# Kernel optimization log

Hardware: AMD Instinct MI355X
Metric: run time of the kernel (lower is better)

The kernel has to match this reference:

```python
import jax, jax.numpy as jnp
import numpy as np

N, E, H, D, F_IN = 50000, 400000, 2, 128, 5
EPS = 1e-5  # BatchNorm eps

def _bn(x, gamma, beta, rm, rv):
    # eval-mode BatchNorm1d using running stats
    return (x - rm) * jax.lax.rsqrt(rv + EPS) * gamma + beta

def setup_inputs() -> dict:
    key = jax.random.key(0)
    ks = jax.random.split(key, 24)
    r = lambda i, shape, s=1.0: jax.random.normal(ks[i], shape, jnp.float32) * s
    u = lambda i, shape: jax.random.uniform(ks[i], shape, jnp.float32)
    return {
        "h": r(0, (N, F_IN)),
        "edge_index": jax.random.randint(ks[1], (2, E), 0, N),
        "edge_weight": r(2, (E, 1)),
        # BatchNorm1d(5)
        "gamma1": 1.0 + r(3, (F_IN,), 0.1), "beta1": r(4, (F_IN,), 0.1),
        "rm1": r(5, (F_IN,), 0.1), "rv1": 0.5 + u(6, (F_IN,)),
        # GATv2Conv params (lin_l, lin_r with bias; lin_edge no bias; att; out bias)
        "Wl": r(7, (F_IN, H * D), 0.2), "bl": r(8, (H * D,), 0.1),
        "Wr": r(9, (F_IN, H * D), 0.2), "br": r(10, (H * D,), 0.1),
        "We": r(11, (1, H * D), 0.2),
        "att": r(12, (H, D), 0.2),
        "bias_gat": r(13, (D,), 0.1),
        # fc1 + BatchNorm1d(128)
        "W1": r(14, (D, D), 0.08), "b1": r(15, (D,), 0.1),
        "gamma2": 1.0 + r(16, (D,), 0.1), "beta2": r(17, (D,), 0.1),
        "rm2": r(18, (D,), 0.1), "rv2": 0.5 + u(19, (D,)),
        # fc2
        "W2": r(20, (D, F_IN), 0.08), "b2": r(21, (F_IN,), 0.1),
    }

def reference(h, edge_index, edge_weight, gamma1, beta1, rm1, rv1,
              Wl, bl, Wr, br, We, att, bias_gat,
              W1, b1, gamma2, beta2, rm2, rv2, W2, b2):
    src, dst = edge_index[0], edge_index[1]
    h = _bn(h, gamma1, beta1, rm1, rv1)
    xl = (h @ Wl + bl).reshape(N, H, D)   # source transform (messages)
    xr = (h @ Wr + br).reshape(N, H, D)   # destination transform
    e = (edge_weight @ We).reshape(E, H, D)
    # GATv2: score = att . leaky_relu(x_j + x_i + edge_emb), slope 0.2
    z = jax.nn.leaky_relu(xl[src] + xr[dst] + e, 0.2)          # [E,H,D]
    logits = jnp.einsum('ehd,hd->eh', z, att)                   # [E,H]
    # segment softmax over edges sharing a destination node
    mx = jax.ops.segment_max(logits, dst, num_segments=N)       # [N,H]
    ex = jnp.exp(logits - mx[dst])
    den = jax.ops.segment_sum(ex, dst, num_segments=N)
    alpha = ex / (den[dst] + 1e-16)                             # [E,H]
    msg = xl[src] * alpha[:, :, None]                           # [E,H,D]
    ssum = jax.ops.segment_sum(msg, dst, num_segments=N)        # [N,H,D]
    cnt = jax.ops.segment_sum(jnp.ones((E,), jnp.float32), dst, num_segments=N)
    out = ssum / jnp.maximum(cnt, 1.0)[:, None, None]           # aggr='mean'
    out = out.mean(axis=1) + bias_gat                           # concat=False -> head mean
    out = out @ W1 + b1
    out = _bn(out, gamma2, beta2, rm2, rv2)
    out = jax.nn.leaky_relu(out, 0.01)
    # dropout is identity in eval mode
    out = out @ W2 + b2                                         # [N,5]
    return out
```

## Files before the change

### kernel.cpp

```cpp
#include <hip/hip_runtime.h>

#define N_NODES 50000
#define N_EDGES 400000
#define F_INP 5
#define HD 256
#define BN_EPS 1e-5f

typedef short v8s __attribute__((ext_vector_type(8)));
typedef float v4f __attribute__((ext_vector_type(4)));
typedef unsigned v4u __attribute__((ext_vector_type(4)));

#define OFF_HBN  0
#define OFF_ACC  400000
#define OFF_BPK  1200000
#define OFF_WF   1202048
#define OFF_W2P  1204096

#define PREP_BLOCKS 3125

#define DPP_ROR_F(x, n) \
    __int_as_float(__builtin_amdgcn_update_dpp(0, __float_as_int(x), 0x120 | (n), 0xF, 0xF, false))

__device__ __forceinline__ unsigned short f2bf(float f) {
    unsigned u = __float_as_uint(f);
    return (unsigned short)((u + 0x7FFFu + ((u >> 16) & 1u)) >> 16);
}
__device__ __forceinline__ unsigned pk2(float a, float b) {
    return (unsigned)f2bf(a) | ((unsigned)f2bf(b) << 16);
}

__device__ __forceinline__ float wcat(int k, int c, const float* Wl, const float* Wr,
                                      const float* We, const float* bl, const float* br) {
    if (k < 5)   return Wl[k * HD + c];
    if (k < 10)  return Wr[(k - 5) * HD + c];
    if (k == 10) return We[c];
    return bl[c] + br[c];
}

__global__ void k_prep(const float* __restrict__ h, const float* __restrict__ g1,
                       const float* __restrict__ be1, const float* __restrict__ rm1,
                       const float* __restrict__ rv1,
                       const float* __restrict__ Wl, const float* __restrict__ bl,
                       const float* __restrict__ Wr, const float* __restrict__ br,
                       const float* __restrict__ We, const float* __restrict__ att,
                       const float* __restrict__ bias_gat,
                       const float* __restrict__ W1, const float* __restrict__ b1,
                       const float* __restrict__ g2, const float* __restrict__ be2,
                       const float* __restrict__ rm2, const float* __restrict__ rv2,
                       const float* __restrict__ W2,
                       float* __restrict__ hbn8, float* __restrict__ acc,
                       unsigned* __restrict__ Bpk,
                       float* __restrict__ Wf, float* __restrict__ W2p) {
    if (blockIdx.x < PREP_BLOCKS) {
        int i = blockIdx.x * blockDim.x + threadIdx.x;
        if (i < N_NODES * 16) acc[i] = 0.f;
        if (i < N_NODES * 8) {
            int f = i & 7, n = i >> 3;
            float v = 0.f;
            if (f < F_INP) {
                float x = h[n * F_INP + f];
                v = (x - rm1[f]) * rsqrtf(rv1[f] + BN_EPS) * g1[f] + be1[f];
            }
            hbn8[i] = v;
        }
        if (i < 1024) {
            int t = i >> 6, l = i & 63;
            int g = l >> 4, c = t * 16 + (l & 15);
            unsigned d0 = 0, d1 = 0;
            if (g < 3) {
                int kb = 4 * g;
                d0 = pk2(wcat(kb + 0, c, Wl, Wr, We, bl, br),
                         wcat(kb + 1, c, Wl, Wr, We, bl, br));
                d1 = pk2(wcat(kb + 2, c, Wl, Wr, We, bl, br),
                         wcat(kb + 3, c, Wl, Wr, We, bl, br));
            }
            Bpk[(t * 64 + l) * 2 + 0] = d0;
            Bpk[(t * 64 + l) * 2 + 1] = d1;
        }
        return;
    }
    int k = blockIdx.x - PREP_BLOCKS;
    int c = threadIdx.x;
    if (c >= 128) return;
    const float* base = (k == 0) ? bl
                      : (k == 1) ? bl + 128
                      : (k < 7)  ? Wl + (k - 2) * HD
                      : (k < 12) ? Wl + (k - 7) * HD + 128
                                 : bias_gat;
    float sum = 0.f;
#pragma unroll 8
    for (int d = 0; d < 128; ++d) sum += base[d] * W1[d * 128 + c];
    if (k == 12) sum += b1[c];
    Wf[c * 16 + k] = sum;
    if (k == 0) {
        float sc = g2[c] * rsqrtf(rv2[c] + BN_EPS);
        Wf[c * 16 + 13] = sc;
        Wf[c * 16 + 14] = be2[c] - rm2[c] * sc;
        Wf[c * 16 + 15] = 0.f;
#pragma unroll
        for (int f = 0; f < 8; ++f)
            W2p[c * 8 + f] = (f < 5) ? W2[c * 5 + f] : 0.f;
    }
}

__launch_bounds__(256)
__global__ void k_edge(const float* __restrict__ hbn8, const int* __restrict__ ei,
                       const float* __restrict__ ew, const unsigned* __restrict__ Bpk,
                       const float* __restrict__ att, float* __restrict__ acc) {
    int lane = threadIdx.x & 63;
    int wv = threadIdx.x >> 6;
    int g = lane >> 4, e16 = lane & 15;

    v8s B[16];
    float AT[16];
#pragma unroll
    for (int t = 0; t < 16; ++t) {
        uint2 d = *(const uint2*)&Bpk[(t * 64 + lane) * 2];
        v4u u = {d.x, d.y, 0u, 0u};
        B[t] = __builtin_bit_cast(v8s, u);
        AT[t] = att[t * 16 + e16];
    }

    int wid = blockIdx.x * 4 + wv;
    int nw = gridDim.x * 4;
    const int NT = N_EDGES / 16;

    int j16 = e16;
    bool sact = j16 < 13;
    int kk = (j16 < 6) ? j16 - 1 : j16 - 7;
    int kc = min(max(kk, 0), 4);

    for (int tile = wid; tile < NT; tile += nw) {
        int e = tile * 16 + e16;
        int src = ei[e];
        int dst = ei[N_EDGES + e];
        float w = ew[e];
        float4 s4 = *(const float4*)&hbn8[src * 8];
        float hs4 = hbn8[src * 8 + 4];
        float4 d4 = *(const float4*)&hbn8[dst * 8];
        float hd4 = hbn8[dst * 8 + 4];

        float a0 = (g == 0) ? s4.x : (g == 1) ? hs4  : d4.w;
        float a1 = (g == 0) ? s4.y : (g == 1) ? d4.x : hd4;
        float a2 = (g == 0) ? s4.z : (g == 1) ? d4.y : w;
        float a3 = (g == 0) ? s4.w : (g == 1) ? d4.z : 1.0f;
        unsigned ua0 = (g < 3) ? pk2(a0, a1) : 0u;
        unsigned ua1 = (g < 3) ? pk2(a2, a3) : 0u;
        v4u uav = {ua0, ua1, 0u, 0u};
        v8s A = __builtin_bit_cast(v8s, uav);

        float p00 = 0.f, p01 = 0.f, p02 = 0.f, p03 = 0.f;
        float p10 = 0.f, p11 = 0.f, p12 = 0.f, p13v = 0.f;
        v4f zero = {0.f, 0.f, 0.f, 0.f};
#pragma unroll
        for (int t = 0; t < 8; ++t) {
            v4f c = __builtin_amdgcn_mfma_f32_16x16x32_bf16(A, B[t], zero, 0, 0, 0);
            p00 += AT[t] * fmaf(0.66666667f, fabsf(c[0]), c[0]);
            p01 += AT[t] * fmaf(0.66666667f, fabsf(c[1]), c[1]);
            p02 += AT[t] * fmaf(0.66666667f, fabsf(c[2]), c[2]);
            p03 += AT[t] * fmaf(0.66666667f, fabsf(c[3]), c[3]);
        }
#pragma unroll
        for (int t = 8; t < 16; ++t) {
            v4f c = __builtin_amdgcn_mfma_f32_16x16x32_bf16(A, B[t], zero, 0, 0, 0);
            p10 += AT[t] * fmaf(0.66666667f, fabsf(c[0]), c[0]);
            p11 += AT[t] * fmaf(0.66666667f, fabsf(c[1]), c[1]);
            p12 += AT[t] * fmaf(0.66666667f, fabsf(c[2]), c[2]);
            p13v += AT[t] * fmaf(0.66666667f, fabsf(c[3]), c[3]);
        }
#pragma unroll
        for (int st = 1; st <= 8; st <<= 1) {
            if (st == 1) {
                p00 += DPP_ROR_F(p00, 1); p01 += DPP_ROR_F(p01, 1);
                p02 += DPP_ROR_F(p02, 1); p03 += DPP_ROR_F(p03, 1);
                p10 += DPP_ROR_F(p10, 1); p11 += DPP_ROR_F(p11, 1);
                p12 += DPP_ROR_F(p12, 1); p13v += DPP_ROR_F(p13v, 1);
            } else if (st == 2) {
                p00 += DPP_ROR_F(p00, 2); p01 += DPP_ROR_F(p01, 2);
                p02 += DPP_ROR_F(p02, 2); p03 += DPP_ROR_F(p03, 2);
                p10 += DPP_ROR_F(p10, 2); p11 += DPP_ROR_F(p11, 2);
                p12 += DPP_ROR_F(p12, 2); p13v += DPP_ROR_F(p13v, 2);
            } else if (st == 4) {
                p00 += DPP_ROR_F(p00, 4); p01 += DPP_ROR_F(p01, 4);
                p02 += DPP_ROR_F(p02, 4); p03 += DPP_ROR_F(p03, 4);
                p10 += DPP_ROR_F(p10, 4); p11 += DPP_ROR_F(p11, 4);
                p12 += DPP_ROR_F(p12, 4); p13v += DPP_ROR_F(p13v, 4);
            } else {
                p00 += DPP_ROR_F(p00, 8); p01 += DPP_ROR_F(p01, 8);
                p02 += DPP_ROR_F(p02, 8); p03 += DPP_ROR_F(p03, 8);
                p10 += DPP_ROR_F(p10, 8); p11 += DPP_ROR_F(p11, 8);
                p12 += DPP_ROR_F(p12, 8); p13v += DPP_ROR_F(p13v, 8);
            }
        }
        float e00 = __expf(0.6f * p00), e01 = __expf(0.6f * p01);
        float e02 = __expf(0.6f * p02), e03 = __expf(0.6f * p03);
        float e10 = __expf(0.6f * p10), e11 = __expf(0.6f * p11);
        float e12 = __expf(0.6f * p12), e13 = __expf(0.6f * p13v);

        if (sact) {
#pragma unroll
            for (int it = 0; it < 4; ++it) {
                int eg = tile * 16 + 4 * g + it;
                int srcg = ei[eg];
                int deg = ei[N_EDGES + eg];
                float hsel = hbn8[srcg * 8 + kc];
                float ex0 = (it == 0) ? e00 : (it == 1) ? e01 : (it == 2) ? e02 : e03;
                float ex1 = (it == 0) ? e10 : (it == 1) ? e11 : (it == 2) ? e12 : e13;
                float base = (j16 < 6) ? ex0 : ex1;
                float v = base * hsel;
                v = (j16 == 0) ? ex0 : v;
                v = (j16 == 6) ? ex1 : v;
                v = (j16 == 12) ? 1.0f : v;
                atomicAdd(&acc[deg * 16 + j16], v);
            }
        }
    }
}

__launch_bounds__(256)
__global__ void k_mlp(const float* __restrict__ acc, const float* __restrict__ Wf,
                      const float* __restrict__ W2p, const float* __restrict__ b2,
                      float* __restrict__ out) {
    int n = blockIdx.x * blockDim.x + threadIdx.x;
    if (n >= N_NODES) return;
    const float* ar = acc + (size_t)n * 16;
    float4 A0 = *(const float4*)(ar + 0);
    float4 A1 = *(const float4*)(ar + 4);
    float4 A2 = *(const float4*)(ar + 8);
    float cnt = ar[12];
    float r0 = 1.f / (A0.x + 1e-16f);
    float r1 = 1.f / (A1.z + 1e-16f);
    float scale = 0.5f / fmaxf(cnt, 1.f);
    float s0 = scale * r0, s1 = scale * r1;
    float m0 = A0.x * s0, m1 = A1.z * s1;
    float m2 = A0.y * s0, m3 = A0.z * s0, m4 = A0.w * s0, m5 = A1.x * s0, m6 = A1.y * s0;
    float m7 = A1.w * s1, m8 = A2.x * s1, m9 = A2.y * s1, m10 = A2.z * s1, m11 = A2.w * s1;

    float o0 = 0.f, o1 = 0.f, o2 = 0.f, o3 = 0.f, o4 = 0.f;
#pragma unroll 4
    for (int c = 0; c < 128; ++c) {
        const float* wr = &Wf[c * 16];
        float a = wr[12];
        a += m0 * wr[0] + m1 * wr[1] + m2 * wr[2] + m3 * wr[3];
        a += m4 * wr[4] + m5 * wr[5] + m6 * wr[6] + m7 * wr[7];
        a += m8 * wr[8] + m9 * wr[9] + m10 * wr[10] + m11 * wr[11];
        a = fmaf(a, wr[13], wr[14]);
        a = fmaxf(a, 0.01f * a);
        const float* w2 = &W2p[c * 8];
        o0 = fmaf(a, w2[0], o0);
        o1 = fmaf(a, w2[1], o1);
        o2 = fmaf(a, w2[2], o2);
        o3 = fmaf(a, w2[3], o3);
        o4 = fmaf(a, w2[4], o4);
    }
    float* op = out + (size_t)n * 5;
    op[0] = o0 + b2[0];
    op[1] = o1 + b2[1];
    op[2] = o2 + b2[2];
    op[3] = o3 + b2[3];
    op[4] = o4 + b2[4];
}

extern "C" void kernel_launch(void* const* d_in, const int* in_sizes, int n_in,
                              void* d_out, int out_size, void* d_ws, size_t ws_size,
                              hipStream_t stream) {
    const float* h    = (const float*)d_in[0];
    const int*   ei   = (const int*)d_in[1];
    const float* ew   = (const float*)d_in[2];
    const float* g1   = (const float*)d_in[3];
    const float* be1  = (const float*)d_in[4];
    const float* rm1  = (const float*)d_in[5];
    const float* rv1  = (const float*)d_in[6];
    const float* Wl   = (const float*)d_in[7];
    const float* bl   = (const float*)d_in[8];
    const float* Wr   = (const float*)d_in[9];
    const float* br   = (const float*)d_in[10];
    const float* We   = (const float*)d_in[11];
    const float* att  = (const float*)d_in[12];
    const float* bias_gat = (const float*)d_in[13];
    const float* W1   = (const float*)d_in[14];
    const float* b1   = (const float*)d_in[15];
    const float* g2   = (const float*)d_in[16];
    const float* be2  = (const float*)d_in[17];
    const float* rm2  = (const float*)d_in[18];
    const float* rv2  = (const float*)d_in[19];
    const float* W2   = (const float*)d_in[20];
    const float* b2   = (const float*)d_in[21];

    float* ws  = (float*)d_ws;
    float* hbn = ws + OFF_HBN;
    float* acc = ws + OFF_ACC;
    unsigned* Bpk = (unsigned*)(ws + OFF_BPK);
    float* Wf  = ws + OFF_WF;
    float* W2p = ws + OFF_W2P;

    k_prep<<<PREP_BLOCKS + 13, 256, 0, stream>>>(
        h, g1, be1, rm1, rv1, Wl, bl, Wr, br, We, att, bias_gat,
        W1, b1, g2, be2, rm2, rv2, W2, hbn, acc, Bpk, Wf, W2p);
    k_edge<<<1280, 256, 0, stream>>>(hbn, ei, ew, Bpk, att, acc);
    k_mlp<<<(N_NODES + 255) / 256, 256, 0, stream>>>(acc, Wf, W2p, b2, (float*)d_out);
}
```

Before: 87.57 us.

## Replicate accumulator buffer per lane group to spread atomic contention

The per-destination accumulator is split into four replicas, and each 16-lane group of a wave atomically adds into its own copy. The MLP kernel sums the four replicas before normalising. The prep kernel now zeroes all replicas with float4 stores, and the edge kernel grid grows from 1280 to 1792 blocks. The aim is to cut same-address atomic contention, at the cost of four times the accumulator zeroing and four times the reads in the MLP.

```diff
diff --git a/kernel.cpp b/kernel.cpp
--- a/kernel.cpp
+++ b/kernel.cpp
@@ -5,6 +5,7 @@
 #define F_INP 5
 #define HD 256
 #define BN_EPS 1e-5f
+#define NREP 4
 
 typedef short v8s __attribute__((ext_vector_type(8)));
 typedef float v4f __attribute__((ext_vector_type(4)));
@@ -12,9 +13,9 @@
 
 #define OFF_HBN  0
 #define OFF_ACC  400000
-#define OFF_BPK  1200000
-#define OFF_WF   1202048
-#define OFF_W2P  1204096
+#define OFF_BPK  3600000
+#define OFF_WF   3602048
+#define OFF_W2P  3604096
 
 #define PREP_BLOCKS 3125
 
@@ -53,7 +54,8 @@
                        float* __restrict__ Wf, float* __restrict__ W2p) {
     if (blockIdx.x < PREP_BLOCKS) {
         int i = blockIdx.x * blockDim.x + threadIdx.x;
-        if (i < N_NODES * 16) acc[i] = 0.f;
+        float4 z = make_float4(0.f, 0.f, 0.f, 0.f);
+        *(float4*)&acc[(size_t)i * 4] = z;
         if (i < N_NODES * 8) {
             int f = i & 7, n = i >> 3;
             float v = 0.f;
@@ -129,6 +131,7 @@
     bool sact = j16 < 13;
     int kk = (j16 < 6) ? j16 - 1 : j16 - 7;
     int kc = min(max(kk, 0), 4);
+    float* accg = acc + (size_t)g * (N_NODES * 16);
 
     for (int tile = wid; tile < NT; tile += nw) {
         int e = tile * 16 + e16;
@@ -168,30 +171,23 @@
             p12 += AT[t] * fmaf(0.66666667f, fabsf(c[2]), c[2]);
             p13v += AT[t] * fmaf(0.66666667f, fabsf(c[3]), c[3]);
         }
-#pragma unroll
-        for (int st = 1; st <= 8; st <<= 1) {
-            if (st == 1) {
-                p00 += DPP_ROR_F(p00, 1); p01 += DPP_ROR_F(p01, 1);
-                p02 += DPP_ROR_F(p02, 1); p03 += DPP_ROR_F(p03, 1);
-                p10 += DPP_ROR_F(p10, 1); p11 += DPP_ROR_F(p11, 1);
-                p12 += DPP_ROR_F(p12, 1); p13v += DPP_ROR_F(p13v, 1);
-            } else if (st == 2) {
-                p00 += DPP_ROR_F(p00, 2); p01 += DPP_ROR_F(p01, 2);
-                p02 += DPP_ROR_F(p02, 2); p03 += DPP_ROR_F(p03, 2);
-                p10 += DPP_ROR_F(p10, 2); p11 += DPP_ROR_F(p11, 2);
-                p12 += DPP_ROR_F(p12, 2); p13v += DPP_ROR_F(p13v, 2);
-            } else if (st == 4) {
-                p00 += DPP_ROR_F(p00, 4); p01 += DPP_ROR_F(p01, 4);
-                p02 += DPP_ROR_F(p02, 4); p03 += DPP_ROR_F(p03, 4);
-                p10 += DPP_ROR_F(p10, 4); p11 += DPP_ROR_F(p11, 4);
-                p12 += DPP_ROR_F(p12, 4); p13v += DPP_ROR_F(p13v, 4);
-            } else {
-                p00 += DPP_ROR_F(p00, 8); p01 += DPP_ROR_F(p01, 8);
-                p02 += DPP_ROR_F(p02, 8); p03 += DPP_ROR_F(p03, 8);
-                p10 += DPP_ROR_F(p10, 8); p11 += DPP_ROR_F(p11, 8);
-                p12 += DPP_ROR_F(p12, 8); p13v += DPP_ROR_F(p13v, 8);
-            }
-        }
+        p00 += DPP_ROR_F(p00, 1); p01 += DPP_ROR_F(p01, 1);
+        p02 += DPP_ROR_F(p02, 1); p03 += DPP_ROR_F(p03, 1);
+        p10 += DPP_ROR_F(p10, 1); p11 += DPP_ROR_F(p11, 1);
+        p12 += DPP_ROR_F(p12, 1); p13v += DPP_ROR_F(p13v, 1);
+        p00 += DPP_ROR_F(p00, 2); p01 += DPP_ROR_F(p01, 2);
+        p02 += DPP_ROR_F(p02, 2); p03 += DPP_ROR_F(p03, 2);
+        p10 += DPP_ROR_F(p10, 2); p11 += DPP_ROR_F(p11, 2);
+        p12 += DPP_ROR_F(p12, 2); p13v += DPP_ROR_F(p13v, 2);
+        p00 += DPP_ROR_F(p00, 4); p01 += DPP_ROR_F(p01, 4);
+        p02 += DPP_ROR_F(p02, 4); p03 += DPP_ROR_F(p03, 4);
+        p10 += DPP_ROR_F(p10, 4); p11 += DPP_ROR_F(p11, 4);
+        p12 += DPP_ROR_F(p12, 4); p13v += DPP_ROR_F(p13v, 4);
+        p00 += DPP_ROR_F(p00, 8); p01 += DPP_ROR_F(p01, 8);
+        p02 += DPP_ROR_F(p02, 8); p03 += DPP_ROR_F(p03, 8);
+        p10 += DPP_ROR_F(p10, 8); p11 += DPP_ROR_F(p11, 8);
+        p12 += DPP_ROR_F(p12, 8); p13v += DPP_ROR_F(p13v, 8);
+
         float e00 = __expf(0.6f * p00), e01 = __expf(0.6f * p01);
         float e02 = __expf(0.6f * p02), e03 = __expf(0.6f * p03);
         float e10 = __expf(0.6f * p10), e11 = __expf(0.6f * p11);
@@ -211,7 +207,7 @@
                 v = (j16 == 0) ? ex0 : v;
                 v = (j16 == 6) ? ex1 : v;
                 v = (j16 == 12) ? 1.0f : v;
-                atomicAdd(&acc[deg * 16 + j16], v);
+                atomicAdd(&accg[deg * 16 + j16], v);
             }
         }
     }
@@ -223,11 +219,21 @@
                       float* __restrict__ out) {
     int n = blockIdx.x * blockDim.x + threadIdx.x;
     if (n >= N_NODES) return;
-    const float* ar = acc + (size_t)n * 16;
-    float4 A0 = *(const float4*)(ar + 0);
-    float4 A1 = *(const float4*)(ar + 4);
-    float4 A2 = *(const float4*)(ar + 8);
-    float cnt = ar[12];
+    float4 A0 = make_float4(0.f, 0.f, 0.f, 0.f);
+    float4 A1 = make_float4(0.f, 0.f, 0.f, 0.f);
+    float4 A2 = make_float4(0.f, 0.f, 0.f, 0.f);
+    float cnt = 0.f;
+#pragma unroll
+    for (int g = 0; g < NREP; ++g) {
+        const float* ar = acc + (size_t)g * (N_NODES * 16) + (size_t)n * 16;
+        float4 B0 = *(const float4*)(ar + 0);
+        float4 B1 = *(const float4*)(ar + 4);
+        float4 B2 = *(const float4*)(ar + 8);
+        A0.x += B0.x; A0.y += B0.y; A0.z += B0.z; A0.w += B0.w;
+        A1.x += B1.x; A1.y += B1.y; A1.z += B1.z; A1.w += B1.w;
+        A2.x += B2.x; A2.y += B2.y; A2.z += B2.z; A2.w += B2.w;
+        cnt += ar[12];
+    }
     float r0 = 1.f / (A0.x + 1e-16f);
     float r1 = 1.f / (A1.z + 1e-16f);
     float scale = 0.5f / fmaxf(cnt, 1.f);
@@ -297,6 +303,6 @@
     k_prep<<<PREP_BLOCKS + 13, 256, 0, stream>>>(
         h, g1, be1, rm1, rv1, Wl, bl, Wr, br, We, att, bias_gat,
         W1, b1, g2, be2, rm2, rv2, W2, hbn, acc, Bpk, Wf, W2p);
-    k_edge<<<1280, 256, 0, stream>>>(hbn, ei, ew, Bpk, att, acc);
+    k_edge<<<1792, 256, 0, stream>>>(hbn, ei, ew, Bpk, att, acc);
     k_mlp<<<(N_NODES + 255) / 256, 256, 0, stream>>>(acc, Wf, W2p, b2, (float*)d_out);
 }
```

Result: slower. 96.91 us, median of 2 (+10.7%).
